# Performance work log

Measured on AMD Instinct MI355X. Metric: run time of the kernel, lower is better.

Reference implementation:

```python
import jax, jax.numpy as jnp
import numpy as np
from jax import lax

NC = 80
REG_MAX = 16
BINS = REG_MAX + 1
RADIUS = 2.5
TOPK = 10
L_BOX, L_CLS, L_DFL = 7.5, 1.0, 1.5


def focal_bce(x, t, alpha=0.25, gamma=2.0):
    # numerically stable BCE-with-logits: max(x,0) - x*t + log1p(exp(-|x|))
    p = jax.nn.sigmoid(x)
    ce = jnp.maximum(x, 0.0) - x * t + jnp.log1p(jnp.exp(-jnp.abs(x)))
    p_t = p * t + (1.0 - p) * (1.0 - t)
    a_t = alpha * t + (1.0 - alpha) * (1.0 - t)
    return ce * a_t * (1.0 - p_t) ** gamma


def _level_loss(reg, cls, boxes, labels, stride):
    B, _, H, W = reg.shape
    HW = H * W
    G = boxes.shape[1]
    gy, gx = jnp.meshgrid(jnp.arange(H, dtype=jnp.float32), jnp.arange(W, dtype=jnp.float32), indexing='ij')
    centers = jnp.stack([gx + 0.5, gy + 0.5], -1).reshape(HW, 2)  # [HW,2]
    gt = boxes / stride  # [B,G,4]
    gctr = (gt[..., :2] + gt[..., 2:]) * 0.5  # [B,G,2]
    cx = centers[None, :, None, 0]
    cy = centers[None, :, None, 1]
    dl = cx - gt[:, None, :, 0]
    dt = cy - gt[:, None, :, 1]
    dr = gt[:, None, :, 2] - cx
    db = gt[:, None, :, 3] - cy
    in_gt = (dl > 0) & (dt > 0) & (dr > 0) & (db > 0)
    in_ctr = ((cx >= gctr[:, None, :, 0] - RADIUS) & (cx <= gctr[:, None, :, 0] + RADIUS)
              & (cy >= gctr[:, None, :, 1] - RADIUS) & (cy <= gctr[:, None, :, 1] + RADIUS))
    mask = in_gt & in_ctr  # [B,HW,G]
    any_pos = jnp.any(mask, axis=(1, 2))  # [B]
    # fallback: topk closest anchor centers per GT (smallest distance along point dim)
    dist = jnp.sqrt(((centers[None, :, None, :] - gctr[:, None, :, :]) ** 2).sum(-1))  # [B,HW,G]
    k = min(TOPK, HW)
    _, idx = lax.top_k(-jnp.swapaxes(dist, 1, 2), k)  # [B,G,k]
    fb = jnp.zeros((B, HW, G), bool).at[jnp.arange(B)[:, None, None], idx, jnp.arange(G)[None, :, None]].set(True)
    mask = jnp.where(any_pos[:, None, None], mask, fb)
    mf = mask.astype(jnp.float32)
    n_pos = mf.sum((1, 2))  # [B] (>=1 by construction of fallback)

    cls_flat = cls.transpose(0, 2, 3, 1).reshape(B, HW, NC)
    reg_flat = reg.transpose(0, 2, 3, 1).reshape(B, HW, 4, BINS)

    # ---- DFL ----
    ltrb = jnp.clip(jnp.stack([dl, dt, dr, db], -1), 0.0)  # [B,HW,G,4]
    tgt = jnp.clip(ltrb, 0.0, REG_MAX - 1e-4)
    lb = jnp.floor(tgt).astype(jnp.int32)
    rb = jnp.minimum(lb + 1, REG_MAX)
    wl = rb.astype(jnp.float32) - tgt
    wr = tgt - lb.astype(jnp.float32)
    logp = jax.nn.log_softmax(reg_flat, -1)  # [B,HW,4,BINS]
    bi = jnp.arange(B)[:, None, None, None]
    pi = jnp.arange(HW)[None, :, None, None]
    ki = jnp.arange(4)[None, None, None, :]
    dfl_pair = -(logp[bi, pi, ki, lb] * wl + logp[bi, pi, ki, rb] * wr)  # [B,HW,G,4]
    dfl = ((dfl_pair * mf[..., None]).sum((1, 2, 3)) / (n_pos * 4.0)).sum()

    # ---- box (IoU, detached as in original) ----
    prob = jax.nn.softmax(reg_flat, -1)
    d = (prob * jnp.arange(BINS, dtype=jnp.float32)).sum(-1)  # [B,HW,4]
    pcx = centers[None, :, 0]
    pcy = centers[None, :, 1]
    pred_box = jnp.stack([pcx - d[..., 0], pcy - d[..., 1], pcx + d[..., 2], pcy + d[..., 3]], -1)  # [B,HW,4]
    b1 = pred_box[:, :, None, :]
    b2 = gt[:, None, :, :]
    iw = jnp.clip(jnp.minimum(b1[..., 2:], b2[..., 2:]) - jnp.maximum(b1[..., :2], b2[..., :2]), 0.0)
    inter = iw[..., 0] * iw[..., 1]
    a1 = (b1[..., 2] - b1[..., 0]) * (b1[..., 3] - b1[..., 1])
    a2 = (b2[..., 2] - b2[..., 0]) * (b2[..., 3] - b2[..., 1])
    iou = lax.stop_gradient(inter / (a1 + a2 - inter + 1e-6))  # [B,HW,G]
    box = ((1.0 - iou) * mf).sum()

    # ---- cls (focal BCE, soft IoU targets). Decompose one-hot target:
    # per positive pair: sum_c f(logit_c,0) - f(logit_cls,0) + f(logit_cls,iou)
    fz = focal_bce(cls_flat, 0.0)  # [B,HW,NC]
    fz_sum = fz.sum(-1)  # [B,HW]
    bi2 = jnp.arange(B)[:, None, None]
    pi2 = jnp.arange(HW)[None, :, None]
    ci = labels[:, None, :]  # [B,1,G]
    cls_at = cls_flat[bi2, pi2, ci]  # [B,HW,G]
    fz_at = fz[bi2, pi2, ci]
    cls_pos = ((fz_sum[:, :, None] - fz_at + focal_bce(cls_at, iou)) * mf).sum()
    pos_pt = jnp.any(mask, -1)  # [B,HW]
    cls_neg = jnp.where(pos_pt, 0.0, fz_sum).sum()
    return box, cls_pos + cls_neg, dfl


def _total(reg0, cls0, reg1, cls1, reg2, cls2, gt_boxes, gt_labels):
    tb = tc = td = 0.0
    for r, c, s in ((reg0, cls0, 8.0), (reg1, cls1, 16.0), (reg2, cls2, 32.0)):
        b, cl, d = _level_loss(r, c, gt_boxes, gt_labels, s)
        tb = tb + b
        tc = tc + cl
        td = td + d
    loss = L_BOX * tb + L_CLS * tc + L_DFL * td
    return loss, tb, tc, td


def setup_inputs() -> dict:
    key = jax.random.key(0)
    ks = jax.random.split(key, 10)
    B, G = 16, 32
    d = {}
    for i, (h, w) in enumerate(((80, 80), (40, 40), (20, 20))):
        d[f'reg{i}'] = jax.random.normal(ks[2 * i], (B, 4 * BINS, h, w), jnp.float32)
        d[f'cls{i}'] = jax.random.normal(ks[2 * i + 1], (B, NC, h, w), jnp.float32)
    ctr = jax.random.uniform(ks[6], (B, G, 2), minval=0.0, maxval=640.0)
    wh = jax.random.uniform(ks[7], (B, G, 2), minval=16.0, maxval=160.0)
    x1y1 = jnp.clip(ctr - wh * 0.5, 0.0, 640.0)
    x2y2 = jnp.clip(ctr + wh * 0.5, 0.0, 640.0)
    d['gt_boxes'] = jnp.concatenate([x1y1, x2y2], -1)
    d['gt_labels'] = jax.random.randint(ks[8], (B, G), 0, NC, jnp.int32)
    return d


def reference(reg0, cls0, reg1, cls1, reg2, cls2, gt_boxes, gt_labels):
    return _total(reg0, cls0, reg1, cls1, reg2, cls2, gt_boxes, gt_labels)
```

## Files before the change

kernel.cpp:

```cpp
#include <hip/hip_runtime.h>
#include <math.h>

#define NCLS 80
#define BINS 17
#define REGMAX 16
#define NG 32
#define NB 16
#define KTOP 10
#define RAD 2.5f

#define WS_ACC   0
#define WS_NPOS  32
#define WS_DFLN  224
#define WS_CNT   608
#define NBLOCKS  (34 * 16)

__device__ __forceinline__ float focal0(float x) {
    float e   = __expf(-fabsf(x));
    float inv = 1.0f / (1.0f + e);
    float p   = (x >= 0.0f) ? inv : e * inv;
    float ce  = fmaxf(x, 0.0f) + __logf(1.0f + e);
    return ce * 0.75f * p * p;
}

__device__ __forceinline__ float focal_t(float x, float t) {
    float e   = __expf(-fabsf(x));
    float inv = 1.0f / (1.0f + e);
    float p   = (x >= 0.0f) ? inv : e * inv;
    float ce  = fmaxf(x, 0.0f) - x * t + __logf(1.0f + e);
    float pt  = p * t + (1.0f - p) * (1.0f - t);
    float at  = 0.25f * t + 0.75f * (1.0f - t);
    float om  = 1.0f - pt;
    return ce * at * om * om;
}

__global__ __launch_bounds__(1024, 8) void k_main_f(
    const float* __restrict__ reg0, const float* __restrict__ cls0,
    const float* __restrict__ reg1, const float* __restrict__ cls1,
    const float* __restrict__ reg2, const float* __restrict__ cls2,
    const float* __restrict__ gtb,  const int* __restrict__ lab,
    float* __restrict__ acc, float* __restrict__ npos, float* __restrict__ dfln,
    int* __restrict__ cnt, float* __restrict__ out)
{
    int bx = blockIdx.x;
    int b  = blockIdx.y;
    int lvl, tix, W; const float *regp, *clsp; float inv_s;
    if (bx < 25)      { lvl = 0; tix = bx;      W = 80; regp = reg0; clsp = cls0; inv_s = 0.125f;   }
    else if (bx < 32) { lvl = 1; tix = bx - 25; W = 40; regp = reg1; clsp = cls1; inv_s = 0.0625f;  }
    else              { lvl = 2; tix = bx - 32; W = 20; regp = reg2; clsp = cls2; inv_s = 0.03125f; }
    int HW = W * W;
    int tile = tix * 256;

    int tid  = threadIdx.x;
    int lane = tid & 63;
    int w    = tid >> 6;
    int p0   = tile + 4 * lane;
    bool v   = p0 < HW;
    int pb   = v ? p0 : HW - 4;

    __shared__ float s_bx[NG][6];
    __shared__ int   s_lab[NG];
    __shared__ float s_dv[4][256], s_lz[4][256], s_fzp[12][256], s_fzs[256];
    __shared__ unsigned char s_ps[16][64];
    __shared__ float red[16][4];
    __shared__ int   s_any, s_tick, s_fb[NG][KTOP];

    if (tid == 0) s_any = 0;
    if (tid < NG) {
        int g = tid;
        float4 bb4 = *(const float4*)(gtb + (b * NG + g) * 4);
        float x1 = bb4.x * inv_s, y1 = bb4.y * inv_s;
        float x2 = bb4.z * inv_s, y2 = bb4.w * inv_s;
        s_bx[g][0] = x1; s_bx[g][1] = y1; s_bx[g][2] = x2; s_bx[g][3] = y2;
        s_bx[g][4] = (x1 + x2) * 0.5f; s_bx[g][5] = (y1 + y2) * 0.5f;
        s_lab[g] = lab[b * NG + g];
    }
    __syncthreads();

    {
        int g = tid >> 5, widx = tid & 31;
        float x1 = s_bx[g][0], y1 = s_bx[g][1];
        float x2 = s_bx[g][2], y2 = s_bx[g][3];
        float gcx = s_bx[g][4], gcy = s_bx[g][5];
        int jc = (int)floorf(gcx), ic = (int)floorf(gcy);
        bool any = false;
#pragma unroll
        for (int r = 0; r < 3; ++r) {
            int ci = widx + 32 * r;
            if (ci < 81) {
                int j = jc + (ci % 9) - 4, i = ic + (ci / 9) - 4;
                if (j >= 0 && j < W && i >= 0 && i < W) {
                    float cx = (float)j + 0.5f, cy = (float)i + 0.5f;
                    bool m = (cx - x1 > 0.0f) && (cy - y1 > 0.0f) &&
                             (x2 - cx > 0.0f) && (y2 - cy > 0.0f) &&
                             (cx >= gcx - RAD) && (cx <= gcx + RAD) &&
                             (cy >= gcy - RAD) && (cy <= gcy + RAD);
                    any = any || m;
                }
            }
        }
        if (__any(any) && (tid & 63) == 0) atomicOr(&s_any, 1);
    }
    __syncthreads();
    bool anyb = s_any != 0;

    if (!anyb) {
        if (tid < NG) {
            int g = tid;
            float gcx = s_bx[g][4], gcy = s_bx[g][5];
            float bd[KTOP]; int bi[KTOP];
            for (int t = 0; t < KTOP; ++t) { bd[t] = 3.0e38f; bi[t] = 0; }
            for (int p = 0; p < HW; ++p) {
                float cx = (float)(p % W) + 0.5f;
                float cy = (float)(p / W) + 0.5f;
                float dx = cx - gcx, dy = cy - gcy;
                float d = dx * dx + dy * dy;
                if (d < bd[KTOP - 1]) {
                    int t = KTOP - 1;
                    while (t > 0 && d < bd[t - 1]) { bd[t] = bd[t-1]; bi[t] = bi[t-1]; --t; }
                    bd[t] = d; bi[t] = p;
                }
            }
            for (int t = 0; t < KTOP; ++t) s_fb[g][t] = bi[t];
        }
        __syncthreads();
    }

    if (w < 4) {
        const float* bp = regp + (size_t)(b * 68 + w * BINS) * HW + pb;
        float m[4], sm[4], ex[4];
#pragma unroll
        for (int j = 0; j < 4; ++j) { m[j] = -3.0e38f; sm[j] = 0.f; ex[j] = 0.f; }
#pragma unroll
        for (int t = 0; t < BINS; ++t) {
            float4 x4 = *(const float4*)(bp + (size_t)t * HW);
            float xv[4] = { x4.x, x4.y, x4.z, x4.w };
#pragma unroll
            for (int j = 0; j < 4; ++j) {
                float nm = fmaxf(m[j], xv[j]);
                float a  = __expf(m[j] - nm);
                float bb = __expf(xv[j] - nm);
                sm[j] = sm[j] * a + bb;
                ex[j] = ex[j] * a + bb * (float)t;
                m[j]  = nm;
            }
        }
        *(float4*)&s_dv[w][4 * lane] =
            make_float4(ex[0] / sm[0], ex[1] / sm[1], ex[2] / sm[2], ex[3] / sm[3]);
        *(float4*)&s_lz[w][4 * lane] =
            make_float4(__logf(sm[0]) + m[0], __logf(sm[1]) + m[1],
                        __logf(sm[2]) + m[2], __logf(sm[3]) + m[3]);
    } else {
        int q  = w - 4;
        int c0 = (q < 10) ? q * 7 : 70 + (q - 10) * 5;
        int nc = (q < 10) ? 7 : 5;
        const float* bp = clsp + (size_t)(b * 80 + c0) * HW + pb;
        float fz[4] = { 0.f, 0.f, 0.f, 0.f };
#pragma unroll
        for (int t = 0; t < 7; ++t) {
            if (t < nc) {
                float4 c4 = *(const float4*)(bp + (size_t)t * HW);
                fz[0] += focal0(c4.x); fz[1] += focal0(c4.y);
                fz[2] += focal0(c4.z); fz[3] += focal0(c4.w);
            }
        }
        *(float4*)&s_fzp[q][4 * lane] = make_float4(fz[0], fz[1], fz[2], fz[3]);
    }
    __syncthreads();

    if (tid < 256) {
        float f = 0.f;
#pragma unroll
        for (int q = 0; q < 12; ++q) f += s_fzp[q][tid];
        s_fzs[tid] = f;
    }
    __syncthreads();

    float bxa = 0.f, cla = 0.f, dfa = 0.f, np = 0.f;
    unsigned posm = 0;
    int ri = p0 / W;
    float cy  = (float)ri + 0.5f;
    float cxb = (float)(p0 - ri * W) + 0.5f;

    if (v) {
        int r0 = tile / W, r1 = min(tile + 255, HW - 1) / W;
        float cyLo = (float)r0 + 0.5f, cyHi = (float)r1 + 0.5f;
#pragma unroll
        for (int gi = 0; gi < 2; ++gi) {
            int g = w + 16 * gi;
            float x1 = s_bx[g][0], y1 = s_bx[g][1];
            float x2 = s_bx[g][2], y2 = s_bx[g][3];
            float gx = s_bx[g][4], gy = s_bx[g][5];
            if (anyb) {
                if (!((cyHi > y1) && (y2 > cyLo) &&
                      (cyHi >= gy - RAD) && (cyLo <= gy + RAD))) continue;
            }
#pragma unroll
            for (int j = 0; j < 4; ++j) {
                float cx = cxb + (float)j;
                float dl = cx - x1, dt = cy - y1, dr = x2 - cx, db = y2 - cy;
                bool mk;
                if (anyb) {
                    mk = (dl > 0.f) && (dt > 0.f) && (dr > 0.f) && (db > 0.f) &&
                         (cx >= gx - RAD) && (cx <= gx + RAD) &&
                         (cy >= gy - RAD) && (cy <= gy + RAD);
                } else {
                    int pt = p0 + j;
                    mk = false;
                    for (int t = 0; t < KTOP; ++t) mk = mk || (s_fb[g][t] == pt);
                }
                if (mk) {
                    posm |= (1u << j);
                    np += 1.f;
                    int ptl = 4 * lane + j, pt = p0 + j;
                    float dv0 = s_dv[0][ptl], dv1 = s_dv[1][ptl];
                    float dv2 = s_dv[2][ptl], dv3 = s_dv[3][ptl];
                    float px1 = cx - dv0, py1 = cy - dv1;
                    float px2 = cx + dv2, py2 = cy + dv3;
                    float pa = (px2 - px1) * (py2 - py1);
                    float ix1 = fmaxf(px1, x1), iy1 = fmaxf(py1, y1);
                    float ix2 = fminf(px2, x2), iy2 = fminf(py2, y2);
                    float iw = fmaxf(ix2 - ix1, 0.f), ih = fmaxf(iy2 - iy1, 0.f);
                    float inter = iw * ih;
                    float ga = (x2 - x1) * (y2 - y1);
                    float iou = inter / (pa + ga - inter + 1e-6f);
                    bxa += 1.f - iou;
                    float ltrb[4] = { dl, dt, dr, db };
#pragma unroll
                    for (int k = 0; k < 4; ++k) {
                        float tt = fminf(fmaxf(ltrb[k], 0.f), 15.9999f);
                        float lf = floorf(tt); int lb = (int)lf;
                        int rb = lb + 1 > REGMAX ? REGMAX : lb + 1;
                        float wl = (float)rb - tt, wr = tt - lf;
                        float lzk = s_lz[k][ptl];
                        float xl = regp[(size_t)(b * 68 + k * BINS + lb) * HW + pt];
                        float xr = regp[(size_t)(b * 68 + k * BINS + rb) * HW + pt];
                        dfa -= (xl - lzk) * wl + (xr - lzk) * wr;
                    }
                    int cc = s_lab[g];
                    float xat = clsp[(size_t)(b * 80 + cc) * HW + pt];
                    cla += s_fzs[ptl] - focal0(xat) + focal_t(xat, iou);
                }
            }
        }
    }
    s_ps[w][lane] = (unsigned char)posm;
    __syncthreads();

    if (tid < 256 && tile + tid < HW) {
        unsigned pg = 0;
#pragma unroll
        for (int wv = 0; wv < 16; ++wv) pg |= s_ps[wv][tid >> 2];
        if (!((pg >> (tid & 3)) & 1u)) cla += s_fzs[tid];
    }

    float v0 = bxa, v1 = cla, v2 = dfa, v3 = np;
    for (int off = 32; off > 0; off >>= 1) {
        v0 += __shfl_down(v0, off);
        v1 += __shfl_down(v1, off);
        v2 += __shfl_down(v2, off);
        v3 += __shfl_down(v3, off);
    }
    if (lane == 0) { red[w][0] = v0; red[w][1] = v1; red[w][2] = v2; red[w][3] = v3; }
    __syncthreads();
    if (tid == 0) {
        float t0 = 0, t1 = 0, t2 = 0, t3 = 0;
        for (int wv = 0; wv < 16; ++wv) {
            t0 += red[wv][0]; t1 += red[wv][1]; t2 += red[wv][2]; t3 += red[wv][3];
        }
        atomicAdd(&acc[0], t0);
        atomicAdd(&acc[1], t1);
        atomicAdd(&dfln[lvl * NB + b], t2);
        atomicAdd(&npos[lvl * NB + b], t3);
    }

    if (tid == 0) {
        __threadfence();
        s_tick = atomicAdd(cnt, 1);
    }
    __syncthreads();
    if (s_tick == NBLOCKS - 1 && tid < 64) {
        float vs = 0.f;
        if (lane < 48) {
            float n = atomicAdd(&npos[lane], 0.0f);
            float d = atomicAdd(&dfln[lane], 0.0f);
            if (n > 0.f) vs = d / (n * 4.0f);
        }
        for (int off = 32; off > 0; off >>= 1) vs += __shfl_down(vs, off);
        if (lane == 0) {
            float tbv = atomicAdd(&acc[0], 0.0f);
            float tcv = atomicAdd(&acc[1], 0.0f);
            out[0] = 7.5f * tbv + tcv + 1.5f * vs;
            out[1] = tbv; out[2] = tcv; out[3] = vs;
        }
    }
}

extern "C" void kernel_launch(void* const* d_in, const int* in_sizes, int n_in,
                              void* d_out, int out_size, void* d_ws, size_t ws_size,
                              hipStream_t stream) {
    const float* reg0 = (const float*)d_in[0];
    const float* cls0 = (const float*)d_in[1];
    const float* reg1 = (const float*)d_in[2];
    const float* cls1 = (const float*)d_in[3];
    const float* reg2 = (const float*)d_in[4];
    const float* cls2 = (const float*)d_in[5];
    const float* gtb  = (const float*)d_in[6];
    const int*   lab  = (const int*)d_in[7];
    float* out = (float*)d_out;

    char*  ws   = (char*)d_ws;
    float* acc  = (float*)(ws + WS_ACC);
    float* npos = (float*)(ws + WS_NPOS);
    float* dfln = (float*)(ws + WS_DFLN);
    int*   cnt  = (int*)(ws + WS_CNT);

    hipMemsetAsync(d_ws, 0, 612, stream);
    k_main_f<<<dim3(34, NB), 1024, 0, stream>>>(reg0, cls0, reg1, cls1, reg2, cls2,
                                                gtb, lab,
                                                acc, npos, dfln, cnt, out);
}
```

Before: 62.75 us.

## Halve tile to 128 points per 512-thread block, doubling grid size

```diff
diff --git a/kernel.cpp b/kernel.cpp
--- a/kernel.cpp
+++ b/kernel.cpp
@@ -13,7 +13,7 @@
 #define WS_NPOS  32
 #define WS_DFLN  224
 #define WS_CNT   608
-#define NBLOCKS  (34 * 16)
+#define NBLOCKS  (67 * 16)
 
 __device__ __forceinline__ float focal0(float x) {
     float e   = __expf(-fabsf(x));
@@ -34,7 +34,7 @@
     return ce * at * om * om;
 }
 
-__global__ __launch_bounds__(1024, 8) void k_main_f(
+__global__ __launch_bounds__(512, 4) void k_main_f(
     const float* __restrict__ reg0, const float* __restrict__ cls0,
     const float* __restrict__ reg1, const float* __restrict__ cls1,
     const float* __restrict__ reg2, const float* __restrict__ cls2,
@@ -45,24 +45,24 @@
     int bx = blockIdx.x;
     int b  = blockIdx.y;
     int lvl, tix, W; const float *regp, *clsp; float inv_s;
-    if (bx < 25)      { lvl = 0; tix = bx;      W = 80; regp = reg0; clsp = cls0; inv_s = 0.125f;   }
-    else if (bx < 32) { lvl = 1; tix = bx - 25; W = 40; regp = reg1; clsp = cls1; inv_s = 0.0625f;  }
-    else              { lvl = 2; tix = bx - 32; W = 20; regp = reg2; clsp = cls2; inv_s = 0.03125f; }
+    if (bx < 50)      { lvl = 0; tix = bx;      W = 80; regp = reg0; clsp = cls0; inv_s = 0.125f;   }
+    else if (bx < 63) { lvl = 1; tix = bx - 50; W = 40; regp = reg1; clsp = cls1; inv_s = 0.0625f;  }
+    else              { lvl = 2; tix = bx - 63; W = 20; regp = reg2; clsp = cls2; inv_s = 0.03125f; }
     int HW = W * W;
-    int tile = tix * 256;
+    int tile = tix * 128;
 
     int tid  = threadIdx.x;
     int lane = tid & 63;
     int w    = tid >> 6;
-    int p0   = tile + 4 * lane;
+    int p0   = tile + 2 * lane;
     bool v   = p0 < HW;
-    int pb   = v ? p0 : HW - 4;
+    int pb   = v ? p0 : HW - 2;
 
     __shared__ float s_bx[NG][6];
     __shared__ int   s_lab[NG];
-    __shared__ float s_dv[4][256], s_lz[4][256], s_fzp[12][256], s_fzs[256];
-    __shared__ unsigned char s_ps[16][64];
-    __shared__ float red[16][4];
+    __shared__ float s_dv[4][128], s_lz[4][128], s_fzp[4][128], s_fzs[128];
+    __shared__ unsigned char s_ps[8][64];
+    __shared__ float red[8][4];
     __shared__ int   s_any, s_tick, s_fb[NG][KTOP];
 
     if (tid == 0) s_any = 0;
@@ -78,15 +78,15 @@
     __syncthreads();
 
     {
-        int g = tid >> 5, widx = tid & 31;
+        int g = tid >> 4, wi = tid & 15;
         float x1 = s_bx[g][0], y1 = s_bx[g][1];
         float x2 = s_bx[g][2], y2 = s_bx[g][3];
         float gcx = s_bx[g][4], gcy = s_bx[g][5];
         int jc = (int)floorf(gcx), ic = (int)floorf(gcy);
         bool any = false;
 #pragma unroll
-        for (int r = 0; r < 3; ++r) {
-            int ci = widx + 32 * r;
+        for (int r = 0; r < 6; ++r) {
+            int ci = wi + 16 * r;
             if (ci < 81) {
                 int j = jc + (ci % 9) - 4, i = ic + (ci / 9) - 4;
                 if (j >= 0 && j < W && i >= 0 && i < W) {
@@ -99,7 +99,7 @@
                 }
             }
         }
-        if (__any(any) && (tid & 63) == 0) atomicOr(&s_any, 1);
+        if (__any(any) && lane == 0) atomicOr(&s_any, 1);
     }
     __syncthreads();
     bool anyb = s_any != 0;
@@ -128,66 +128,55 @@
 
     if (w < 4) {
         const float* bp = regp + (size_t)(b * 68 + w * BINS) * HW + pb;
-        float m[4], sm[4], ex[4];
-#pragma unroll
-        for (int j = 0; j < 4; ++j) { m[j] = -3.0e38f; sm[j] = 0.f; ex[j] = 0.f; }
+        float m0 = -3.0e38f, m1 = -3.0e38f, s0 = 0.f, s1 = 0.f, e0 = 0.f, e1 = 0.f;
+        float2 cur = *(const float2*)bp;
 #pragma unroll
         for (int t = 0; t < BINS; ++t) {
-            float4 x4 = *(const float4*)(bp + (size_t)t * HW);
-            float xv[4] = { x4.x, x4.y, x4.z, x4.w };
-#pragma unroll
-            for (int j = 0; j < 4; ++j) {
-                float nm = fmaxf(m[j], xv[j]);
-                float a  = __expf(m[j] - nm);
-                float bb = __expf(xv[j] - nm);
-                sm[j] = sm[j] * a + bb;
-                ex[j] = ex[j] * a + bb * (float)t;
-                m[j]  = nm;
-            }
-        }
-        *(float4*)&s_dv[w][4 * lane] =
-            make_float4(ex[0] / sm[0], ex[1] / sm[1], ex[2] / sm[2], ex[3] / sm[3]);
-        *(float4*)&s_lz[w][4 * lane] =
-            make_float4(__logf(sm[0]) + m[0], __logf(sm[1]) + m[1],
-                        __logf(sm[2]) + m[2], __logf(sm[3]) + m[3]);
+            float2 nxt = (t < BINS - 1) ? *(const float2*)(bp + (size_t)(t + 1) * HW)
+                                        : make_float2(0.f, 0.f);
+            float nm0 = fmaxf(m0, cur.x);
+            float a0  = __expf(m0 - nm0), b0 = __expf(cur.x - nm0);
+            s0 = s0 * a0 + b0; e0 = e0 * a0 + b0 * (float)t; m0 = nm0;
+            float nm1 = fmaxf(m1, cur.y);
+            float a1  = __expf(m1 - nm1), b1 = __expf(cur.y - nm1);
+            s1 = s1 * a1 + b1; e1 = e1 * a1 + b1 * (float)t; m1 = nm1;
+            cur = nxt;
+        }
+        s_dv[w][2*lane]   = e0 / s0;  s_lz[w][2*lane]   = __logf(s0) + m0;
+        s_dv[w][2*lane+1] = e1 / s1;  s_lz[w][2*lane+1] = __logf(s1) + m1;
     } else {
-        int q  = w - 4;
-        int c0 = (q < 10) ? q * 7 : 70 + (q - 10) * 5;
-        int nc = (q < 10) ? 7 : 5;
-        const float* bp = clsp + (size_t)(b * 80 + c0) * HW + pb;
-        float fz[4] = { 0.f, 0.f, 0.f, 0.f };
-#pragma unroll
-        for (int t = 0; t < 7; ++t) {
-            if (t < nc) {
-                float4 c4 = *(const float4*)(bp + (size_t)t * HW);
-                fz[0] += focal0(c4.x); fz[1] += focal0(c4.y);
-                fz[2] += focal0(c4.z); fz[3] += focal0(c4.w);
-            }
-        }
-        *(float4*)&s_fzp[q][4 * lane] = make_float4(fz[0], fz[1], fz[2], fz[3]);
-    }
-    __syncthreads();
-
-    if (tid < 256) {
-        float f = 0.f;
-#pragma unroll
-        for (int q = 0; q < 12; ++q) f += s_fzp[q][tid];
-        s_fzs[tid] = f;
-    }
+        int q = w - 4;
+        const float* bp = clsp + (size_t)(b * 80 + q * 20) * HW + pb;
+        float fz0 = 0.f, fz1 = 0.f;
+#pragma unroll
+        for (int t = 0; t < 20; t += 4) {
+            float2 c0 = *(const float2*)(bp + (size_t)(t    ) * HW);
+            float2 c1 = *(const float2*)(bp + (size_t)(t + 1) * HW);
+            float2 c2 = *(const float2*)(bp + (size_t)(t + 2) * HW);
+            float2 c3 = *(const float2*)(bp + (size_t)(t + 3) * HW);
+            fz0 += focal0(c0.x) + focal0(c1.x) + focal0(c2.x) + focal0(c3.x);
+            fz1 += focal0(c0.y) + focal0(c1.y) + focal0(c2.y) + focal0(c3.y);
+        }
+        s_fzp[q][2*lane] = fz0; s_fzp[q][2*lane+1] = fz1;
+    }
+    __syncthreads();
+
+    if (tid < 128)
+        s_fzs[tid] = s_fzp[0][tid] + s_fzp[1][tid] + s_fzp[2][tid] + s_fzp[3][tid];
     __syncthreads();
 
     float bxa = 0.f, cla = 0.f, dfa = 0.f, np = 0.f;
     unsigned posm = 0;
     int ri = p0 / W;
     float cy  = (float)ri + 0.5f;
-    float cxb = (float)(p0 - ri * W) + 0.5f;
+    float cx0 = (float)(p0 - ri * W) + 0.5f;
 
     if (v) {
-        int r0 = tile / W, r1 = min(tile + 255, HW - 1) / W;
+        int r0 = tile / W, r1 = min(tile + 127, HW - 1) / W;
         float cyLo = (float)r0 + 0.5f, cyHi = (float)r1 + 0.5f;
 #pragma unroll
-        for (int gi = 0; gi < 2; ++gi) {
-            int g = w + 16 * gi;
+        for (int gi = 0; gi < 4; ++gi) {
+            int g = w + 8 * gi;
             float x1 = s_bx[g][0], y1 = s_bx[g][1];
             float x2 = s_bx[g][2], y2 = s_bx[g][3];
             float gx = s_bx[g][4], gy = s_bx[g][5];
@@ -196,8 +185,8 @@
                       (cyHi >= gy - RAD) && (cyLo <= gy + RAD))) continue;
             }
 #pragma unroll
-            for (int j = 0; j < 4; ++j) {
-                float cx = cxb + (float)j;
+            for (int j = 0; j < 2; ++j) {
+                float cx = cx0 + (float)j;
                 float dl = cx - x1, dt = cy - y1, dr = x2 - cx, db = y2 - cy;
                 bool mk;
                 if (anyb) {
@@ -212,7 +201,7 @@
                 if (mk) {
                     posm |= (1u << j);
                     np += 1.f;
-                    int ptl = 4 * lane + j, pt = p0 + j;
+                    int ptl = 2 * lane + j, pt = p0 + j;
                     float dv0 = s_dv[0][ptl], dv1 = s_dv[1][ptl];
                     float dv2 = s_dv[2][ptl], dv3 = s_dv[3][ptl];
                     float px1 = cx - dv0, py1 = cy - dv1;
@@ -247,11 +236,11 @@
     s_ps[w][lane] = (unsigned char)posm;
     __syncthreads();
 
-    if (tid < 256 && tile + tid < HW) {
+    if (tid < 128 && tile + tid < HW) {
         unsigned pg = 0;
 #pragma unroll
-        for (int wv = 0; wv < 16; ++wv) pg |= s_ps[wv][tid >> 2];
-        if (!((pg >> (tid & 3)) & 1u)) cla += s_fzs[tid];
+        for (int wv = 0; wv < 8; ++wv) pg |= s_ps[wv][tid >> 1];
+        if (!((pg >> (tid & 1)) & 1u)) cla += s_fzs[tid];
     }
 
     float v0 = bxa, v1 = cla, v2 = dfa, v3 = np;
@@ -265,7 +254,7 @@
     __syncthreads();
     if (tid == 0) {
         float t0 = 0, t1 = 0, t2 = 0, t3 = 0;
-        for (int wv = 0; wv < 16; ++wv) {
+        for (int wv = 0; wv < 8; ++wv) {
             t0 += red[wv][0]; t1 += red[wv][1]; t2 += red[wv][2]; t3 += red[wv][3];
         }
         atomicAdd(&acc[0], t0);
@@ -316,7 +305,7 @@
     int*   cnt  = (int*)(ws + WS_CNT);
 
     hipMemsetAsync(d_ws, 0, 612, stream);
-    k_main_f<<<dim3(34, NB), 1024, 0, stream>>>(reg0, cls0, reg1, cls1, reg2, cls2,
-                                                gtb, lab,
-                                                acc, npos, dfln, cnt, out);
+    k_main_f<<<dim3(67, NB), 512, 0, stream>>>(reg0, cls0, reg1, cls1, reg2, cls2,
+                                               gtb, lab,
+                                               acc, npos, dfln, cnt, out);
 }
```

After: 65.35 us. 1.04x slower.

## Halve block size, batch all loads per wave, two-pass softmax for DFL

Applied to the files above, without the earlier changes.

```diff
diff --git a/kernel.cpp b/kernel.cpp
--- a/kernel.cpp
+++ b/kernel.cpp
@@ -34,7 +34,7 @@
     return ce * at * om * om;
 }
 
-__global__ __launch_bounds__(1024, 8) void k_main_f(
+__global__ __launch_bounds__(512, 2) void k_main_f(
     const float* __restrict__ reg0, const float* __restrict__ cls0,
     const float* __restrict__ reg1, const float* __restrict__ cls1,
     const float* __restrict__ reg2, const float* __restrict__ cls2,
@@ -60,9 +60,9 @@
 
     __shared__ float s_bx[NG][6];
     __shared__ int   s_lab[NG];
-    __shared__ float s_dv[4][256], s_lz[4][256], s_fzp[12][256], s_fzs[256];
-    __shared__ unsigned char s_ps[16][64];
-    __shared__ float red[16][4];
+    __shared__ float s_dv[4][256], s_lz[4][256], s_fzp[4][256], s_fzs[256];
+    __shared__ unsigned char s_ps[8][64];
+    __shared__ float red[8][4];
     __shared__ int   s_any, s_tick, s_fb[NG][KTOP];
 
     if (tid == 0) s_any = 0;
@@ -78,15 +78,15 @@
     __syncthreads();
 
     {
-        int g = tid >> 5, widx = tid & 31;
+        int g = tid >> 4, wi = tid & 15;
         float x1 = s_bx[g][0], y1 = s_bx[g][1];
         float x2 = s_bx[g][2], y2 = s_bx[g][3];
         float gcx = s_bx[g][4], gcy = s_bx[g][5];
         int jc = (int)floorf(gcx), ic = (int)floorf(gcy);
         bool any = false;
 #pragma unroll
-        for (int r = 0; r < 3; ++r) {
-            int ci = widx + 32 * r;
+        for (int r = 0; r < 6; ++r) {
+            int ci = wi + 16 * r;
             if (ci < 81) {
                 int j = jc + (ci % 9) - 4, i = ic + (ci / 9) - 4;
                 if (j >= 0 && j < W && i >= 0 && i < W) {
@@ -99,7 +99,7 @@
                 }
             }
         }
-        if (__any(any) && (tid & 63) == 0) atomicOr(&s_any, 1);
+        if (__any(any) && lane == 0) atomicOr(&s_any, 1);
     }
     __syncthreads();
     bool anyb = s_any != 0;
@@ -128,21 +128,28 @@
 
     if (w < 4) {
         const float* bp = regp + (size_t)(b * 68 + w * BINS) * HW + pb;
+        float4 rv[BINS];
+#pragma unroll
+        for (int t = 0; t < BINS; ++t)
+            rv[t] = *(const float4*)(bp + (size_t)t * HW);
+        asm volatile("s_waitcnt vmcnt(0)" ::: "memory");
+        __builtin_amdgcn_sched_barrier(0);
         float m[4], sm[4], ex[4];
 #pragma unroll
         for (int j = 0; j < 4; ++j) { m[j] = -3.0e38f; sm[j] = 0.f; ex[j] = 0.f; }
 #pragma unroll
         for (int t = 0; t < BINS; ++t) {
-            float4 x4 = *(const float4*)(bp + (size_t)t * HW);
-            float xv[4] = { x4.x, x4.y, x4.z, x4.w };
+            float xv[4] = { rv[t].x, rv[t].y, rv[t].z, rv[t].w };
+#pragma unroll
+            for (int j = 0; j < 4; ++j) m[j] = fmaxf(m[j], xv[j]);
+        }
+#pragma unroll
+        for (int t = 0; t < BINS; ++t) {
+            float xv[4] = { rv[t].x, rv[t].y, rv[t].z, rv[t].w };
 #pragma unroll
             for (int j = 0; j < 4; ++j) {
-                float nm = fmaxf(m[j], xv[j]);
-                float a  = __expf(m[j] - nm);
-                float bb = __expf(xv[j] - nm);
-                sm[j] = sm[j] * a + bb;
-                ex[j] = ex[j] * a + bb * (float)t;
-                m[j]  = nm;
+                float e = __expf(xv[j] - m[j]);
+                sm[j] += e; ex[j] += e * (float)t;
             }
         }
         *(float4*)&s_dv[w][4 * lane] =
@@ -151,29 +158,26 @@
             make_float4(__logf(sm[0]) + m[0], __logf(sm[1]) + m[1],
                         __logf(sm[2]) + m[2], __logf(sm[3]) + m[3]);
     } else {
-        int q  = w - 4;
-        int c0 = (q < 10) ? q * 7 : 70 + (q - 10) * 5;
-        int nc = (q < 10) ? 7 : 5;
-        const float* bp = clsp + (size_t)(b * 80 + c0) * HW + pb;
+        int q = w - 4;
+        const float* bp = clsp + (size_t)(b * 80 + q * 20) * HW + pb;
+        float4 cv[20];
+#pragma unroll
+        for (int t = 0; t < 20; ++t)
+            cv[t] = *(const float4*)(bp + (size_t)t * HW);
+        asm volatile("s_waitcnt vmcnt(0)" ::: "memory");
+        __builtin_amdgcn_sched_barrier(0);
         float fz[4] = { 0.f, 0.f, 0.f, 0.f };
 #pragma unroll
-        for (int t = 0; t < 7; ++t) {
-            if (t < nc) {
-                float4 c4 = *(const float4*)(bp + (size_t)t * HW);
-                fz[0] += focal0(c4.x); fz[1] += focal0(c4.y);
-                fz[2] += focal0(c4.z); fz[3] += focal0(c4.w);
-            }
+        for (int t = 0; t < 20; ++t) {
+            fz[0] += focal0(cv[t].x); fz[1] += focal0(cv[t].y);
+            fz[2] += focal0(cv[t].z); fz[3] += focal0(cv[t].w);
         }
         *(float4*)&s_fzp[q][4 * lane] = make_float4(fz[0], fz[1], fz[2], fz[3]);
     }
     __syncthreads();
 
-    if (tid < 256) {
-        float f = 0.f;
-#pragma unroll
-        for (int q = 0; q < 12; ++q) f += s_fzp[q][tid];
-        s_fzs[tid] = f;
-    }
+    if (tid < 256)
+        s_fzs[tid] = s_fzp[0][tid] + s_fzp[1][tid] + s_fzp[2][tid] + s_fzp[3][tid];
     __syncthreads();
 
     float bxa = 0.f, cla = 0.f, dfa = 0.f, np = 0.f;
@@ -186,8 +190,8 @@
         int r0 = tile / W, r1 = min(tile + 255, HW - 1) / W;
         float cyLo = (float)r0 + 0.5f, cyHi = (float)r1 + 0.5f;
 #pragma unroll
-        for (int gi = 0; gi < 2; ++gi) {
-            int g = w + 16 * gi;
+        for (int gi = 0; gi < 4; ++gi) {
+            int g = w + 8 * gi;
             float x1 = s_bx[g][0], y1 = s_bx[g][1];
             float x2 = s_bx[g][2], y2 = s_bx[g][3];
             float gx = s_bx[g][4], gy = s_bx[g][5];
@@ -250,7 +254,7 @@
     if (tid < 256 && tile + tid < HW) {
         unsigned pg = 0;
 #pragma unroll
-        for (int wv = 0; wv < 16; ++wv) pg |= s_ps[wv][tid >> 2];
+        for (int wv = 0; wv < 8; ++wv) pg |= s_ps[wv][tid >> 2];
         if (!((pg >> (tid & 3)) & 1u)) cla += s_fzs[tid];
     }
 
@@ -265,7 +269,7 @@
     __syncthreads();
     if (tid == 0) {
         float t0 = 0, t1 = 0, t2 = 0, t3 = 0;
-        for (int wv = 0; wv < 16; ++wv) {
+        for (int wv = 0; wv < 8; ++wv) {
             t0 += red[wv][0]; t1 += red[wv][1]; t2 += red[wv][2]; t3 += red[wv][3];
         }
         atomicAdd(&acc[0], t0);
@@ -316,7 +320,7 @@
     int*   cnt  = (int*)(ws + WS_CNT);
 
     hipMemsetAsync(d_ws, 0, 612, stream);
-    k_main_f<<<dim3(34, NB), 1024, 0, stream>>>(reg0, cls0, reg1, cls1, reg2, cls2,
-                                                gtb, lab,
-                                                acc, npos, dfln, cnt, out);
+    k_main_f<<<dim3(34, NB), 512, 0, stream>>>(reg0, cls0, reg1, cls1, reg2, cls2,
+                                               gtb, lab,
+                                               acc, npos, dfln, cnt, out);
 }
```

Result: faster. 58.69 us (-6.5%).
